# Performance work log

Hardware: AMD Instinct MI355X
Metric: run time of the kernel (lower is better)

Reference implementation:

```python
import jax, jax.numpy as jnp
import numpy as np

B, T, J, D = 64, 2048, 128, 512


def setup_inputs() -> dict:
    key = jax.random.key(0)
    k1, k2, k3, k4 = jax.random.split(key, 4)
    question = jax.random.normal(k1, (B, J, D), dtype=jnp.float32)
    context = jax.random.normal(k2, (B, T, D), dtype=jnp.float32)
    question_len = jax.random.randint(k3, (B,), 1, J + 1, dtype=jnp.int32)
    context_len = jax.random.randint(k4, (B,), 1, T + 1, dtype=jnp.int32)
    weight = jnp.ones((D, 1), dtype=jnp.float32)  # initializer='ones'
    return {"question": question, "context": context,
            "question_len": question_len, "context_len": context_len,
            "weight": weight}


def reference(question, context, question_len, context_len, weight):
    # Original computes sum_d context[b,t,d]*question[b,j,d]*w[d] via a
    # broadcast [B,T,J,D] intermediate; reformulated as a batched GEMM.
    w = weight[:, 0]                                   # [D]
    sim = jnp.einsum('btd,bjd->btj', context * w, question)  # [B,T,J]
    Jm = question.shape[1]
    Tm = context.shape[1]
    q_mask = (jnp.arange(Jm) < question_len[:, None]).astype(jnp.float32)  # [B,J]
    c_mask = (jnp.arange(Tm) < context_len[:, None]).astype(jnp.float32)   # [B,T]
    mask = c_mask[:, :, None] * q_mask[:, None, :]     # [B,T,J]
    neg = jnp.finfo(jnp.float32).min
    sim = sim + neg * (1.0 - mask)
    attn = jax.nn.softmax(sim, axis=1)                 # softmax over context axis T
    return jnp.sum(attn * mask, axis=2)[..., None]     # [B,T,1]
```

## Files before the change

### kernel.cpp

```cpp
#include <hip/hip_runtime.h>
#include <math.h>

#define BB 64
#define TT 2048
#define JJ 128
#define DD 512
#define BK 32

typedef short short8 __attribute__((ext_vector_type(8)));
typedef float f32x4 __attribute__((ext_vector_type(4)));

__device__ inline unsigned pk_hi(float a, float b) {
  return __builtin_amdgcn_perm(__float_as_uint(b), __float_as_uint(a), 0x07060302u);
}
__device__ inline float truncbf(float x) {
  return __uint_as_float(__float_as_uint(x) & 0xFFFF0000u);
}
__device__ inline void pack8(float4 a, float4 b, uint4& h, uint4& l) {
  h = make_uint4(pk_hi(a.x, a.y), pk_hi(a.z, a.w), pk_hi(b.x, b.y), pk_hi(b.z, b.w));
  float l0 = a.x - truncbf(a.x), l1 = a.y - truncbf(a.y);
  float l2 = a.z - truncbf(a.z), l3 = a.w - truncbf(a.w);
  float l4 = b.x - truncbf(b.x), l5 = b.y - truncbf(b.y);
  float l6 = b.z - truncbf(b.z), l7 = b.w - truncbf(b.w);
  l = make_uint4(pk_hi(l0, l1), pk_hi(l2, l3), pk_hi(l4, l5), pk_hi(l6, l7));
}
__device__ inline short8 bc8(uint4 u) { return __builtin_bit_cast(short8, u); }

__global__ __launch_bounds__(256, 3)
void sim_gemm_mfma(const float* __restrict__ Qm, const float* __restrict__ Cm,
                   const float* __restrict__ w, float* __restrict__ S) {
  __shared__ uint4 Ahi[128 * 4];
  __shared__ uint4 Alo[128 * 4];
  __shared__ uint4 Bhi[128 * 4];
  __shared__ uint4 Blo[128 * 4];

  const int tid = threadIdx.x;
  const int b = blockIdx.y;
  const int t0 = blockIdx.x * 128;

  const int sr = tid >> 1;
  const int sc0 = (tid & 1) * 2;
  const int ssw = (sr >> 1) & 3;
  const int slotA0 = sr * 4 + (sc0 ^ ssw);
  const int slotA1 = sr * 4 + ((sc0 + 1) ^ ssw);

  const float* qp = Qm + ((size_t)b * JJ + sr) * DD + sc0 * 8;
  const float* cp = Cm + ((size_t)b * TT + t0 + sr) * DD + sc0 * 8;
  const float* wp = w + sc0 * 8;

  const int lane = tid & 63;
  const int wv = tid >> 6;
  const int wm = (wv & 1) * 64;
  const int wn = (wv >> 1) * 64;
  const int l15 = lane & 15;
  const int q = lane >> 4;
  const int fchunk = q ^ ((l15 >> 1) & 3);

  int aslot[4], bslot[4];
#pragma unroll
  for (int i = 0; i < 4; i++) {
    aslot[i] = (wm + i * 16 + l15) * 4 + fchunk;
    bslot[i] = (wn + i * 16 + l15) * 4 + fchunk;
  }

  f32x4 acc[4][4] = {};

  for (int ks = 0; ks < 16; ks++) {
    const int k0 = ks * BK;
    float4 q0 = *(const float4*)(qp + k0 + 0);
    float4 q1 = *(const float4*)(qp + k0 + 4);
    float4 q2 = *(const float4*)(qp + k0 + 8);
    float4 q3 = *(const float4*)(qp + k0 + 12);
    float4 w0 = *(const float4*)(wp + k0 + 0);
    float4 w1 = *(const float4*)(wp + k0 + 4);
    float4 w2 = *(const float4*)(wp + k0 + 8);
    float4 w3 = *(const float4*)(wp + k0 + 12);
    float4 c0 = *(const float4*)(cp + k0 + 0);
    float4 c1 = *(const float4*)(cp + k0 + 4);
    float4 c2 = *(const float4*)(cp + k0 + 8);
    float4 c3 = *(const float4*)(cp + k0 + 12);
    q0.x *= w0.x; q0.y *= w0.y; q0.z *= w0.z; q0.w *= w0.w;
    q1.x *= w1.x; q1.y *= w1.y; q1.z *= w1.z; q1.w *= w1.w;
    q2.x *= w2.x; q2.y *= w2.y; q2.z *= w2.z; q2.w *= w2.w;
    q3.x *= w3.x; q3.y *= w3.y; q3.z *= w3.z; q3.w *= w3.w;

    __syncthreads();
    uint4 h, l;
    pack8(q0, q1, h, l); Ahi[slotA0] = h; Alo[slotA0] = l;
    pack8(q2, q3, h, l); Ahi[slotA1] = h; Alo[slotA1] = l;
    pack8(c0, c1, h, l); Bhi[slotA0] = h; Blo[slotA0] = l;
    pack8(c2, c3, h, l); Bhi[slotA1] = h; Blo[slotA1] = l;
    __syncthreads();

    short8 bh[4], bl[4];
#pragma unroll
    for (int ni = 0; ni < 4; ni++) {
      bh[ni] = bc8(Bhi[bslot[ni]]);
      bl[ni] = bc8(Blo[bslot[ni]]);
    }
#pragma unroll
    for (int mi = 0; mi < 4; mi++) {
      short8 ah = bc8(Ahi[aslot[mi]]);
      short8 al = bc8(Alo[aslot[mi]]);
#pragma unroll
      for (int ni = 0; ni < 4; ni++) {
        acc[mi][ni] = __builtin_amdgcn_mfma_f32_16x16x32_bf16(ah, bh[ni], acc[mi][ni], 0, 0, 0);
        acc[mi][ni] = __builtin_amdgcn_mfma_f32_16x16x32_bf16(al, bh[ni], acc[mi][ni], 0, 0, 0);
        acc[mi][ni] = __builtin_amdgcn_mfma_f32_16x16x32_bf16(ah, bl[ni], acc[mi][ni], 0, 0, 0);
      }
    }
  }

#pragma unroll
  for (int mi = 0; mi < 4; mi++) {
#pragma unroll
    for (int ni = 0; ni < 4; ni++) {
      const int j = wm + mi * 16 + q * 4;
      const int t = t0 + wn + ni * 16 + l15;
      float* dst = S + ((size_t)b * JJ + j) * TT + t;
      dst[0 * TT] = acc[mi][ni][0];
      dst[1 * TT] = acc[mi][ni][1];
      dst[2 * TT] = acc[mi][ni][2];
      dst[3 * TT] = acc[mi][ni][3];
    }
  }
}

__global__ __launch_bounds__(256)
void softmax_stats_kernel(const float* __restrict__ S, const int* __restrict__ qlen,
                          const int* __restrict__ clen, float* __restrict__ m_out,
                          float* __restrict__ r_out) {
  const int j = blockIdx.x;
  const int b = blockIdx.y;
  if (j >= qlen[b]) return;
  const int cl = clen[b];
  const int tid = threadIdx.x;
  const float4* row = (const float4*)(S + ((size_t)b * JJ + j) * TT);

  float4 v0 = row[tid];
  float4 v1 = row[tid + 256];
  const int t0 = tid * 4;
  const int t1 = (tid + 256) * 4;
  const float NEG = -3.4e38f;

  float m = NEG;
  m = fmaxf(m, (t0 + 0 < cl) ? v0.x : NEG);
  m = fmaxf(m, (t0 + 1 < cl) ? v0.y : NEG);
  m = fmaxf(m, (t0 + 2 < cl) ? v0.z : NEG);
  m = fmaxf(m, (t0 + 3 < cl) ? v0.w : NEG);
  m = fmaxf(m, (t1 + 0 < cl) ? v1.x : NEG);
  m = fmaxf(m, (t1 + 1 < cl) ? v1.y : NEG);
  m = fmaxf(m, (t1 + 2 < cl) ? v1.z : NEG);
  m = fmaxf(m, (t1 + 3 < cl) ? v1.w : NEG);

  __shared__ float red[8];
#pragma unroll
  for (int off = 32; off > 0; off >>= 1) m = fmaxf(m, __shfl_down(m, off));
  if ((tid & 63) == 0) red[tid >> 6] = m;
  __syncthreads();
  m = fmaxf(fmaxf(red[0], red[1]), fmaxf(red[2], red[3]));

  float s = 0.f;
  s += (t0 + 0 < cl) ? __expf(v0.x - m) : 0.f;
  s += (t0 + 1 < cl) ? __expf(v0.y - m) : 0.f;
  s += (t0 + 2 < cl) ? __expf(v0.z - m) : 0.f;
  s += (t0 + 3 < cl) ? __expf(v0.w - m) : 0.f;
  s += (t1 + 0 < cl) ? __expf(v1.x - m) : 0.f;
  s += (t1 + 1 < cl) ? __expf(v1.y - m) : 0.f;
  s += (t1 + 2 < cl) ? __expf(v1.z - m) : 0.f;
  s += (t1 + 3 < cl) ? __expf(v1.w - m) : 0.f;
#pragma unroll
  for (int off = 32; off > 0; off >>= 1) s += __shfl_down(s, off);
  if ((tid & 63) == 0) red[4 + (tid >> 6)] = s;
  __syncthreads();
  s = red[4] + red[5] + red[6] + red[7];

  if (tid == 0) {
    m_out[(size_t)b * JJ + j] = m;
    r_out[(size_t)b * JJ + j] = 1.f / s;
  }
}

__global__ __launch_bounds__(256)
void out_kernel(const float* __restrict__ S, const float* __restrict__ m_arr,
                const float* __restrict__ r_arr, const int* __restrict__ qlen,
                const int* __restrict__ clen, float* __restrict__ out) {
  const int b = blockIdx.y;
  const int t = blockIdx.x * 256 + threadIdx.x;
  const int ql = qlen[b];
  const int cl = clen[b];

  __shared__ float lm[JJ];
  __shared__ float lr[JJ];
  if (threadIdx.x < ql) {
    lm[threadIdx.x] = m_arr[(size_t)b * JJ + threadIdx.x];
    lr[threadIdx.x] = r_arr[(size_t)b * JJ + threadIdx.x];
  }
  __syncthreads();

  float acc = 0.f;
  if (t < cl) {
    const float* col = S + (size_t)b * JJ * TT + t;
#pragma unroll 4
    for (int j = 0; j < ql; j++) {
      acc += __expf(col[(size_t)j * TT] - lm[j]) * lr[j];
    }
  }
  out[(size_t)b * TT + t] = acc;
}

extern "C" void kernel_launch(void* const* d_in, const int* in_sizes, int n_in,
                              void* d_out, int out_size, void* d_ws, size_t ws_size,
                              hipStream_t stream) {
  const float* question = (const float*)d_in[0];
  const float* context  = (const float*)d_in[1];
  const int*   qlen     = (const int*)d_in[2];
  const int*   clen     = (const int*)d_in[3];
  const float* weight   = (const float*)d_in[4];
  float* out = (float*)d_out;

  float* S = (float*)d_ws;
  float* m_arr = S + (size_t)BB * JJ * TT;
  float* r_arr = m_arr + (size_t)BB * JJ;

  sim_gemm_mfma<<<dim3(TT / 128, BB), 256, 0, stream>>>(question, context, weight, S);
  softmax_stats_kernel<<<dim3(JJ, BB), 256, 0, stream>>>(S, qlen, clen, m_arr, r_arr);
  out_kernel<<<dim3(TT / 256, BB), 256, 0, stream>>>(S, m_arr, r_arr, qlen, clen, out);
}
```

Before: 445.7 us.

## Load question fragments directly into registers and prefetch context tiles

Drops the shared-memory staging of the question (A) operand. Each lane now loads its own MFMA fragment of question from global memory, scales it by the weight and splits it into bf16 hi/lo inside the inner loop. Context tiles are software-prefetched one k-step ahead into registers, which halves LDS use and lets global loads overlap the MFMAs. The cost is redundant global loads of question across the two waves sharing the same rows, plus extra VALU pack work on the MFMA path.

```diff
diff --git a/kernel.cpp b/kernel.cpp
--- a/kernel.cpp
+++ b/kernel.cpp
@@ -5,7 +5,6 @@
 #define TT 2048
 #define JJ 128
 #define DD 512
-#define BK 32
 
 typedef short short8 __attribute__((ext_vector_type(8)));
 typedef float f32x4 __attribute__((ext_vector_type(4)));
@@ -29,8 +28,6 @@
 __global__ __launch_bounds__(256, 3)
 void sim_gemm_mfma(const float* __restrict__ Qm, const float* __restrict__ Cm,
                    const float* __restrict__ w, float* __restrict__ S) {
-  __shared__ uint4 Ahi[128 * 4];
-  __shared__ uint4 Alo[128 * 4];
   __shared__ uint4 Bhi[128 * 4];
   __shared__ uint4 Blo[128 * 4];
 
@@ -39,14 +36,11 @@
   const int t0 = blockIdx.x * 128;
 
   const int sr = tid >> 1;
-  const int sc0 = (tid & 1) * 2;
+  const int h = tid & 1;
   const int ssw = (sr >> 1) & 3;
-  const int slotA0 = sr * 4 + (sc0 ^ ssw);
-  const int slotA1 = sr * 4 + ((sc0 + 1) ^ ssw);
-
-  const float* qp = Qm + ((size_t)b * JJ + sr) * DD + sc0 * 8;
-  const float* cp = Cm + ((size_t)b * TT + t0 + sr) * DD + sc0 * 8;
-  const float* wp = w + sc0 * 8;
+  const int slot0 = sr * 4 + ((2 * h + 0) ^ ssw);
+  const int slot1 = sr * 4 + ((2 * h + 1) ^ ssw);
+  const float* cp = Cm + ((size_t)b * TT + t0 + sr) * DD + h * 16;
 
   const int lane = tid & 63;
   const int wv = tid >> 6;
@@ -56,41 +50,39 @@
   const int q = lane >> 4;
   const int fchunk = q ^ ((l15 >> 1) & 3);
 
-  int aslot[4], bslot[4];
-#pragma unroll
-  for (int i = 0; i < 4; i++) {
-    aslot[i] = (wm + i * 16 + l15) * 4 + fchunk;
-    bslot[i] = (wn + i * 16 + l15) * 4 + fchunk;
-  }
+  int bslot[4];
+#pragma unroll
+  for (int i = 0; i < 4; i++) bslot[i] = (wn + i * 16 + l15) * 4 + fchunk;
+
+  const float* qrow = Qm + ((size_t)b * JJ + wm + l15) * DD + q * 8;
+  const float* wp = w + q * 8;
 
   f32x4 acc[4][4] = {};
 
+  float4 c0 = *(const float4*)(cp + 0);
+  float4 c1 = *(const float4*)(cp + 4);
+  float4 c2 = *(const float4*)(cp + 8);
+  float4 c3 = *(const float4*)(cp + 12);
+
   for (int ks = 0; ks < 16; ks++) {
-    const int k0 = ks * BK;
-    float4 q0 = *(const float4*)(qp + k0 + 0);
-    float4 q1 = *(const float4*)(qp + k0 + 4);
-    float4 q2 = *(const float4*)(qp + k0 + 8);
-    float4 q3 = *(const float4*)(qp + k0 + 12);
-    float4 w0 = *(const float4*)(wp + k0 + 0);
-    float4 w1 = *(const float4*)(wp + k0 + 4);
-    float4 w2 = *(const float4*)(wp + k0 + 8);
-    float4 w3 = *(const float4*)(wp + k0 + 12);
-    float4 c0 = *(const float4*)(cp + k0 + 0);
-    float4 c1 = *(const float4*)(cp + k0 + 4);
-    float4 c2 = *(const float4*)(cp + k0 + 8);
-    float4 c3 = *(const float4*)(cp + k0 + 12);
-    q0.x *= w0.x; q0.y *= w0.y; q0.z *= w0.z; q0.w *= w0.w;
-    q1.x *= w1.x; q1.y *= w1.y; q1.z *= w1.z; q1.w *= w1.w;
-    q2.x *= w2.x; q2.y *= w2.y; q2.z *= w2.z; q2.w *= w2.w;
-    q3.x *= w3.x; q3.y *= w3.y; q3.z *= w3.z; q3.w *= w3.w;
-
+    const int k0 = ks * 32;
     __syncthreads();
-    uint4 h, l;
-    pack8(q0, q1, h, l); Ahi[slotA0] = h; Alo[slotA0] = l;
-    pack8(q2, q3, h, l); Ahi[slotA1] = h; Alo[slotA1] = l;
-    pack8(c0, c1, h, l); Bhi[slotA0] = h; Blo[slotA0] = l;
-    pack8(c2, c3, h, l); Bhi[slotA1] = h; Blo[slotA1] = l;
+    {
+      uint4 hh, ll;
+      pack8(c0, c1, hh, ll);
+      Bhi[slot0] = hh; Blo[slot0] = ll;
+      pack8(c2, c3, hh, ll);
+      Bhi[slot1] = hh; Blo[slot1] = ll;
+    }
+    const int kn = (ks < 15) ? k0 + 32 : 0;
+    c0 = *(const float4*)(cp + kn + 0);
+    c1 = *(const float4*)(cp + kn + 4);
+    c2 = *(const float4*)(cp + kn + 8);
+    c3 = *(const float4*)(cp + kn + 12);
     __syncthreads();
+
+    const float4 w0 = *(const float4*)(wp + k0);
+    const float4 w1 = *(const float4*)(wp + k0 + 4);
 
     short8 bh[4], bl[4];
 #pragma unroll
@@ -98,10 +90,17 @@
       bh[ni] = bc8(Bhi[bslot[ni]]);
       bl[ni] = bc8(Blo[bslot[ni]]);
     }
+
 #pragma unroll
     for (int mi = 0; mi < 4; mi++) {
-      short8 ah = bc8(Ahi[aslot[mi]]);
-      short8 al = bc8(Alo[aslot[mi]]);
+      const float* qp = qrow + (size_t)(mi * 16) * DD + k0;
+      float4 va = *(const float4*)(qp);
+      float4 vb = *(const float4*)(qp + 4);
+      va.x *= w0.x; va.y *= w0.y; va.z *= w0.z; va.w *= w0.w;
+      vb.x *= w1.x; vb.y *= w1.y; vb.z *= w1.z; vb.w *= w1.w;
+      uint4 ah4, al4;
+      pack8(va, vb, ah4, al4);
+      short8 ah = bc8(ah4), al = bc8(al4);
 #pragma unroll
       for (int ni = 0; ni < 4; ni++) {
         acc[mi][ni] = __builtin_amdgcn_mfma_f32_16x16x32_bf16(ah, bh[ni], acc[mi][ni], 0, 0, 0);
```

Result: slower. 464.6 us (+4.2%).
